# Kernel optimization log

Hardware: AMD Instinct MI355X
Metric: run time of the kernel (lower is better)

The kernel has to match this reference:

```python
import jax, jax.numpy as jnp
import numpy as np
import math

HEAD_DIM = 64
NQ = 24          # num query heads
NKV = 4          # num kv heads
HIDDEN = 1536
WINDOW = 256     # sliding window (layer_idx=0 -> active)
THETA = 10000.0
EPS = 1e-6


def _rope(x, cos, sin):
    # x: [B,S,H,D]; cos/sin: [S,1,D//2]  (broadcast over B and heads)
    xr = x.reshape(*x.shape[:-1], -1, 2)
    x1, x2 = xr[..., 0], xr[..., 1]
    r = jnp.stack([x1 * cos - x2 * sin, x2 * cos + x1 * sin], axis=-1)
    return r.reshape(x.shape)


def setup_inputs() -> dict:
    key = jax.random.key(0)
    k1, k2, k3 = jax.random.split(key, 3)
    B, S = 2, 2048
    x = jax.random.normal(k1, (B, S, HIDDEN), dtype=jnp.float32)
    norm_scale = jnp.ones((HIDDEN,), dtype=jnp.float32)             # RMSNorm scale
    w_qkv = jax.random.normal(k2, ((NQ + 2 * NKV) * HEAD_DIM, HIDDEN), dtype=jnp.float32) * 0.02
    w_out = jax.random.normal(k3, (HIDDEN, NQ * HEAD_DIM), dtype=jnp.float32) * 0.02
    return {"x": x, "norm_scale": norm_scale, "w_qkv": w_qkv, "w_out": w_out, "start_pos": 0}


def reference(x, norm_scale, w_qkv, w_out, start_pos):
    B, S, _ = x.shape
    # RMSNorm
    var = jnp.mean(x * x, axis=-1, keepdims=True)
    xn = x * jax.lax.rsqrt(var + EPS) * norm_scale
    # QKV projection (nn.Linear: x @ W^T)
    qkv = xn @ w_qkv.T
    qs, kvs = NQ * HEAD_DIM, NKV * HEAD_DIM
    q = qkv[..., :qs].reshape(B, S, NQ, HEAD_DIM)
    k = qkv[..., qs:qs + kvs].reshape(B, S, NKV, HEAD_DIM)
    v = qkv[..., qs + kvs:].reshape(B, S, NKV, HEAD_DIM)
    # RoPE
    inv_freq = 1.0 / (THETA ** (jnp.arange(0, HEAD_DIM, 2, dtype=jnp.float32) / HEAD_DIM))
    t = jnp.arange(start_pos, start_pos + S, dtype=jnp.float32)
    freqs = t[:, None] * inv_freq[None, :]                       # [S, D//2]
    cos, sin = jnp.cos(freqs)[:, None, :], jnp.sin(freqs)[:, None, :]
    q = _rope(q, cos, sin)
    k = _rope(k, cos, sin)
    # GQA: expand kv heads (repeat_interleave over head dim)
    rep = NQ // NKV
    k = jnp.repeat(k, rep, axis=2)
    v = jnp.repeat(v, rep, axis=2)
    # attention with causal + sliding-window mask
    scale = 1.0 / math.sqrt(HEAD_DIM)
    scores = jnp.einsum('bqhd,bkhd->bhqk', q * scale, k)        # [B,H,S,S]
    ipos = start_pos + jnp.arange(S)
    j = jnp.arange(S)
    mask = (j[None, :] > ipos[:, None]) | (j[None, :] < ipos[:, None] - WINDOW)
    scores = jnp.where(mask[None, None], -jnp.inf, scores)
    probs = jax.nn.softmax(scores, axis=-1)
    attn = jnp.einsum('bhqk,bkhd->bqhd', probs, v).reshape(B, S, NQ * HEAD_DIM)
    # output projection + residual
    return x + attn @ w_out.T
```

## Files before the change

kernel.cpp:

```cpp
#include <hip/hip_runtime.h>
#include <hip/hip_bf16.h>

typedef float f32x4 __attribute__((ext_vector_type(4)));
typedef short s16x8 __attribute__((ext_vector_type(8)));
typedef unsigned short u16;

#define B_ 2
#define S_ 2048
#define HID 1536
#define NQ_ 24
#define NKV_ 4
#define HD 64
#define NTOK (B_*S_)
#define QKVN ((NQ_+2*NKV_)*HD)
#define ROPE_BLOCKS ((NTOK*28*32)/256)
#define VT_BLOCKS (B_*NKV_*(S_/64))

#define LDS_FENCE() asm volatile("" ::: "memory")

#define WAITBAR(n) asm volatile("s_waitcnt vmcnt(" #n ")\n\ts_barrier" ::: "memory")
#define RAWBAR()   asm volatile("s_barrier" ::: "memory")

__device__ __forceinline__ float bf2f(u16 u) {
  unsigned int x = ((unsigned int)u) << 16;
  float f; __builtin_memcpy(&f, &x, 4); return f;
}
__device__ __forceinline__ u16 f2bf(float f) {
  unsigned int u; __builtin_memcpy(&u, &f, 4);
  u += 0x7fffu + ((u >> 16) & 1u);
  return (u16)(u >> 16);
}
__device__ __forceinline__ unsigned long long pk4bf(float a, float b, float c, float d) {
  __hip_bfloat162 x = __float22bfloat162_rn(make_float2(a, b));
  __hip_bfloat162 y = __float22bfloat162_rn(make_float2(c, d));
  unsigned int xi, yi;
  __builtin_memcpy(&xi, &x, 4);
  __builtin_memcpy(&yi, &y, 4);
  return (unsigned long long)xi | ((unsigned long long)yi << 32);
}

__global__ __launch_bounds__(256) void k_cvt2(const float* __restrict__ s0, int n0q,
                                              const float* __restrict__ s1, int n1q,
                                              u16* __restrict__ dst) {
  int i = blockIdx.x * 256 + threadIdx.x;
  if (i >= n0q + n1q) return;
  const float* src = (i < n0q) ? s0 : s1;
  int j = (i < n0q) ? i : i - n0q;
  f32x4 v = ((const f32x4*)src)[j];
  *(unsigned long long*)(dst + (size_t)i*4) = pk4bf(v[0], v[1], v[2], v[3]);
}

__global__ __launch_bounds__(384) void k_rmsnorm(const float* __restrict__ x,
                                                 const float* __restrict__ g,
                                                 u16* __restrict__ xn) {
  int row = blockIdx.x;
  int t = threadIdx.x;
  f32x4 v = ((const f32x4*)(x + (size_t)row * HID))[t];
  float ss = v[0]*v[0] + v[1]*v[1] + v[2]*v[2] + v[3]*v[3];
#pragma unroll
  for (int off = 1; off < 64; off <<= 1) ss += __shfl_xor(ss, off);
  __shared__ float red[6];
  if ((t & 63) == 0) red[t >> 6] = ss;
  __syncthreads();
  float tot = red[0] + red[1] + red[2] + red[3] + red[4] + red[5];
  float rs = rsqrtf(tot * (1.f/HID) + 1e-6f);
  f32x4 gv = ((const f32x4*)g)[t];
  ((unsigned long long*)(xn + (size_t)row * HID))[t] =
      pk4bf(v[0]*rs*gv[0], v[1]*rs*gv[1], v[2]*rs*gv[2], v[3]*rs*gv[3]);
}

template <bool F32OUT>
__global__ __launch_bounds__(256) void k_gemm_bt(const u16* __restrict__ A,
                                                 const u16* __restrict__ W,
                                                 void* __restrict__ Cv,
                                                 const float* __restrict__ resid,
                                                 int N, int K) {
  __shared__ __align__(16) u16 As0[128*64], Bs0[64*64];
  __shared__ __align__(16) u16 As1[128*64], Bs1[64*64];
  int lin = blockIdx.x;
  int xcd = lin & 7, loc = lin >> 3;
  int mloc = loc & 3, nloc = loc >> 2;
  int m0 = (xcd*4 + mloc) * 128, n0 = nloc * 64;
  int tid = threadIdx.x;
  int w = tid >> 6, l = tid & 63;
  int wr = w >> 1, wc = w & 1;
  int c = l & 15, g = l >> 4;
  f32x4 acc[4][2] = {};
  int r8 = l >> 3;
  int sslot = (l & 7) ^ r8;
  const u16* Ag = A + (size_t)(m0 + w*32 + r8)*K + sslot*8;
  const u16* Wg = W + (size_t)(n0 + w*16 + r8)*K + sslot*8;

#define STAGE(dA, dB, k0) do {                                                          \
  _Pragma("unroll")                                                                     \
  for (int i = 0; i < 4; i++)                                                           \
    __builtin_amdgcn_global_load_lds(                                                   \
        (const __attribute__((address_space(1))) void*)(Ag + (size_t)(i*8)*K + (k0)),   \
        (__attribute__((address_space(3))) void*)(dA + (w*32 + i*8)*64), 16, 0, 0);     \
  _Pragma("unroll")                                                                     \
  for (int i = 0; i < 2; i++)                                                           \
    __builtin_amdgcn_global_load_lds(                                                   \
        (const __attribute__((address_space(1))) void*)(Wg + (size_t)(i*8)*K + (k0)),   \
        (__attribute__((address_space(3))) void*)(dB + (w*16 + i*8)*64), 16, 0, 0);     \
  } while (0)

#define COMPUTE(sA, sB) do {                                                            \
  _Pragma("unroll")                                                                     \
  for (int ks = 0; ks < 2; ks++) {                                                      \
    s16x8 af[4], bq[2];                                                                 \
    int sl = ((ks*4 + g) ^ (c & 7)) * 8;                                                \
    _Pragma("unroll")                                                                   \
    for (int mt = 0; mt < 4; mt++)                                                      \
      af[mt] = *(const s16x8*)(sA + (wr*64 + mt*16 + c)*64 + sl);                       \
    _Pragma("unroll")                                                                   \
    for (int nt = 0; nt < 2; nt++)                                                      \
      bq[nt] = *(const s16x8*)(sB + (wc*32 + nt*16 + c)*64 + sl);                       \
    _Pragma("unroll")                                                                   \
    for (int mt = 0; mt < 4; mt++)                                                      \
      _Pragma("unroll")                                                                 \
      for (int nt = 0; nt < 2; nt++)                                                    \
        acc[mt][nt] = __builtin_amdgcn_mfma_f32_16x16x32_bf16(af[mt], bq[nt],           \
                                                              acc[mt][nt], 0, 0, 0);    \
  } } while (0)

  const int NT = K >> 6;
  STAGE(As0, Bs0, 0);
  STAGE(As1, Bs1, 64);
  WAITBAR(6);
  for (int t = 0; t + 2 < NT; t += 2) {
    COMPUTE(As0, Bs0);
    RAWBAR();
    STAGE(As0, Bs0, (t+2)*64);
    WAITBAR(6);
    COMPUTE(As1, Bs1);
    RAWBAR();
    if (t + 3 < NT) {
      STAGE(As1, Bs1, (t+3)*64);
      WAITBAR(6);
    } else {
      WAITBAR(0);
    }
  }
  COMPUTE(As0, Bs0);
  WAITBAR(0);
  COMPUTE(As1, Bs1);
#undef STAGE
#undef COMPUTE

#pragma unroll
  for (int mt = 0; mt < 4; mt++)
#pragma unroll
    for (int nt = 0; nt < 2; nt++)
#pragma unroll
      for (int r = 0; r < 4; r++) {
        int m = m0 + wr*64 + mt*16 + g*4 + r;
        int n = n0 + wc*32 + nt*16 + c;
        size_t off = (size_t)m*N + n;
        float vv = acc[mt][nt][r];
        if (F32OUT) {
          ((float*)Cv)[off] = vv + resid[off];
        } else {
          ((u16*)Cv)[off] = f2bf(vv);
        }
      }
}

__global__ __launch_bounds__(256) void k_rope_vt(const u16* __restrict__ qkv,
                                                 u16* __restrict__ q,
                                                 u16* __restrict__ k,
                                                 u16* __restrict__ vt,
                                                 const int* __restrict__ spp) {
  __shared__ u16 tile[64][65];
  int bid = blockIdx.x;
  if (bid < ROPE_BLOCKS) {
    int idx = bid * 256 + threadIdx.x;
    int p = idx & 31;
    int h = (idx >> 5) % 28;
    int tok = idx / 896;
    int s = tok & (S_ - 1);
    int b = tok >> 11;
    float t = (float)(spp[0] + s);
    float inv = exp2f((float)p * -0.41524101186f);
    float fr = t * inv;
    float sn, cs;
    sincosf(fr, &sn, &cs);
    int col = (h < NQ_) ? h*64 + 2*p : HID + (h - NQ_)*64 + 2*p;
    unsigned int pr = *(const unsigned int*)(qkv + (size_t)tok*QKVN + col);
    float x1 = bf2f((u16)(pr & 0xffff));
    float x2 = bf2f((u16)(pr >> 16));
    float y1 = x1*cs - x2*sn;
    float y2 = x2*cs + x1*sn;
    unsigned int outp = (unsigned int)f2bf(y1) | ((unsigned int)f2bf(y2) << 16);
    if (h < NQ_) {
      *(unsigned int*)(q + (((size_t)(b*NQ_ + h))*S_ + s)*64 + 2*p) = outp;
    } else {
      *(unsigned int*)(k + (((size_t)(b*NKV_ + (h - NQ_)))*S_ + s)*64 + 2*p) = outp;
    }
  } else {
    int blk = bid - ROPE_BLOCKS;
    int st = blk & 31;
    int hk = (blk >> 5) & 3;
    int b = blk >> 7;
    int s0 = st * 64;
#pragma unroll
    for (int i = 0; i < 16; i++) {
      int ii = threadIdx.x + i*256;
      int r = ii >> 6, cc = ii & 63;
      tile[r][cc] = qkv[((size_t)(b*S_) + s0 + r)*QKVN + (NQ_+NKV_)*64 + hk*64 + cc];
    }
    __syncthreads();
#pragma unroll
    for (int i = 0; i < 16; i++) {
      int ii = threadIdx.x + i*256;
      int d = ii >> 6, s = ii & 63;
      vt[((size_t)(b*NKV_ + hk)*64 + d)*S_ + s0 + s] = tile[s][d];
    }
  }
}

__global__ __launch_bounds__(64, 3) void k_attn(const u16* __restrict__ q,
                                                const u16* __restrict__ k,
                                                const u16* __restrict__ vt,
                                                u16* __restrict__ ao,
                                                const int* __restrict__ spp) {
  __shared__ __align__(16) u16 Pt[32*72];
  int lin = blockIdx.x;
  int xcd = lin & 7, loc = lin >> 3;
  int qb = loc & 63;
  int bh = xcd * 6 + (loc >> 6);
  int h = bh % NQ_;
  int b = bh / NQ_;
  int q0 = qb * 32;
  int hk = h / (NQ_/NKV_);
  int l = threadIdx.x;
  int c = l & 15, g = l >> 4;
  int sp = spp[0];
  const u16* qptr = q + ((size_t)(b*NQ_ + h))*S_*64;
  const u16* kptr = k + ((size_t)(b*NKV_ + hk))*S_*64;
  const u16* vptr = vt + ((size_t)(b*NKV_ + hk))*64*S_;

  s16x8 qf[2][2];
#pragma unroll
  for (int qt = 0; qt < 2; qt++)
#pragma unroll
    for (int ks = 0; ks < 2; ks++)
      qf[qt][ks] = *(const s16x8*)(qptr + (size_t)(q0 + qt*16 + c)*64 + ks*32 + g*8);

  f32x4 o[4][2] = {};
  float m_run[2], l_run[2];
#pragma unroll
  for (int i = 0; i < 2; i++) { m_run[i] = -1e30f; l_run[i] = 0.f; }

  int lo = sp + q0 - 256; if (lo < 0) lo = 0;
  int hi = sp + q0 + 31;  if (hi > S_ - 1) hi = S_ - 1;
  int kt0 = lo >> 6, kt1 = hi >> 6;

  s16x8 kf[4][2];
#pragma unroll
  for (int km = 0; km < 4; km++)
#pragma unroll
    for (int ks = 0; ks < 2; ks++)
      kf[km][ks] = *(const s16x8*)(kptr + (size_t)(kt0*64 + km*16 + c)*64 + ks*32 + g*8);

  for (int kt = kt0; kt <= kt1; kt++) {
    s16x8 vf[2][4];
#pragma unroll
    for (int ks = 0; ks < 2; ks++)
#pragma unroll
      for (int dt = 0; dt < 4; dt++)
        vf[ks][dt] = *(const s16x8*)(vptr + (size_t)(dt*16 + c)*S_ + kt*64 + ks*32 + g*8);

    bool full = (kt*64 + 63 <= sp + q0) && (kt*64 >= sp + q0 - 225);
#pragma unroll
    for (int qt = 0; qt < 2; qt++) {
      f32x4 sa[4];
      __builtin_amdgcn_s_setprio(1);
#pragma unroll
      for (int km = 0; km < 4; km++) {
        f32x4 z = {};
        z = __builtin_amdgcn_mfma_f32_16x16x32_bf16(kf[km][0], qf[qt][0], z, 0, 0, 0);
        sa[km] = __builtin_amdgcn_mfma_f32_16x16x32_bf16(kf[km][1], qf[qt][1], z, 0, 0, 0);
      }
      __builtin_amdgcn_s_setprio(0);
      if (qt == 1 && kt < kt1) {
#pragma unroll
        for (int km = 0; km < 4; km++)
#pragma unroll
          for (int ks = 0; ks < 2; ks++)
            kf[km][ks] = *(const s16x8*)(kptr + (size_t)((kt+1)*64 + km*16 + c)*64 + ks*32 + g*8);
      }
      float mx = -1e30f;
      if (full) {
#pragma unroll
        for (int km = 0; km < 4; km++)
#pragma unroll
          for (int r = 0; r < 4; r++) {
            float sv = sa[km][r] * 0.125f;
            sa[km][r] = sv;
            mx = fmaxf(mx, sv);
          }
      } else {
        int pos = sp + q0 + qt*16 + c;
#pragma unroll
        for (int km = 0; km < 4; km++)
#pragma unroll
          for (int r = 0; r < 4; r++) {
            int key = kt*64 + km*16 + g*4 + r;
            float sv = sa[km][r] * 0.125f;
            sv = ((unsigned)(pos - key) <= 256u) ? sv : -1e30f;
            sa[km][r] = sv;
            mx = fmaxf(mx, sv);
          }
      }
      mx = fmaxf(mx, __shfl_xor(mx, 16));
      mx = fmaxf(mx, __shfl_xor(mx, 32));
      float mnew = fmaxf(m_run[qt], mx);
      float alpha = __expf(m_run[qt] - mnew);
      m_run[qt] = mnew;
      float rsum = 0.f;
#pragma unroll
      for (int km = 0; km < 4; km++) {
        float p0 = __expf(sa[km][0] - mnew);
        float p1 = __expf(sa[km][1] - mnew);
        float p2 = __expf(sa[km][2] - mnew);
        float p3 = __expf(sa[km][3] - mnew);
        rsum += p0 + p1 + p2 + p3;
        *(unsigned long long*)(Pt + (qt*16 + c)*72 + km*16 + g*4) = pk4bf(p0, p1, p2, p3);
      }
      rsum += __shfl_xor(rsum, 16);
      rsum += __shfl_xor(rsum, 32);
      l_run[qt] = l_run[qt]*alpha + rsum;
#pragma unroll
      for (int dt = 0; dt < 4; dt++) {
        o[dt][qt][0] *= alpha; o[dt][qt][1] *= alpha;
        o[dt][qt][2] *= alpha; o[dt][qt][3] *= alpha;
      }
    }
    LDS_FENCE();
    __builtin_amdgcn_s_setprio(1);
#pragma unroll
    for (int ks = 0; ks < 2; ks++)
#pragma unroll
      for (int qt = 0; qt < 2; qt++) {
        s16x8 pf = *(const s16x8*)(Pt + (qt*16 + c)*72 + ks*32 + g*8);
#pragma unroll
        for (int dt = 0; dt < 4; dt++)
          o[dt][qt] = __builtin_amdgcn_mfma_f32_16x16x32_bf16(vf[ks][dt], pf, o[dt][qt], 0, 0, 0);
      }
    __builtin_amdgcn_s_setprio(0);
    LDS_FENCE();
  }
#pragma unroll
  for (int qt = 0; qt < 2; qt++) {
    float inv = 1.f / l_run[qt];
    int qi = q0 + qt*16 + c;
    u16* row = ao + ((size_t)(b*S_) + qi)*HID + h*64;
#pragma unroll
    for (int dt = 0; dt < 4; dt++)
      *(unsigned long long*)(row + dt*16 + g*4) =
          pk4bf(o[dt][qt][0]*inv, o[dt][qt][1]*inv, o[dt][qt][2]*inv, o[dt][qt][3]*inv);
  }
}

extern "C" void kernel_launch(void* const* d_in, const int* in_sizes, int n_in,
                              void* d_out, int out_size, void* d_ws, size_t ws_size,
                              hipStream_t stream) {
  const float* x_f32    = (const float*)d_in[0];
  const float* g_f32    = (const float*)d_in[1];
  const float* wqkv_f32 = (const float*)d_in[2];
  const float* wout_f32 = (const float*)d_in[3];
  const int*   spp      = (const int*)d_in[4];
  char* ws = (char*)d_ws;
  u16* wqkvb = (u16*)(ws);
  u16* woutb = (u16*)(ws + 6291456);
  u16* xn    = (u16*)(ws + 11010048);
  u16* qkv   = (u16*)(ws + 23592960);
  u16* qbuf  = (u16*)(ws + 40370176);
  u16* kbuf  = (u16*)(ws + 52953088);
  u16* vtb   = (u16*)(ws + 55050240);
  u16* attn  = xn;

  const int nwq4 = QKVN*HID/4, nwo4 = HID*HID/4;
  k_cvt2<<<(nwq4 + nwo4 + 255)/256, 256, 0, stream>>>(wqkv_f32, nwq4, wout_f32, nwo4, wqkvb);
  k_rmsnorm<<<NTOK, 384, 0, stream>>>(x_f32, g_f32, xn);
  k_gemm_bt<false><<<32*(QKVN/64), 256, 0, stream>>>(xn, wqkvb, qkv, nullptr, QKVN, HID);
  k_rope_vt<<<ROPE_BLOCKS + VT_BLOCKS, 256, 0, stream>>>(qkv, qbuf, kbuf, vtb, spp);
  k_attn<<<B_*NQ_*(S_/32), 64, 0, stream>>>(qbuf, kbuf, vtb, attn, spp);
  k_gemm_bt<true><<<32*(HID/64), 256, 0, stream>>>(attn, woutb, d_out, x_f32, HID, HID);
}
```

Measured before the change: 208.7 us.

## Merge setup kernels and precompute RoPE cos/sin table for vectorized rope

Weight conversion, RMSNorm and a new cos/sin table computation now run as one setup kernel, which removes a launch. The RoPE kernel reads precomputed cos/sin pairs from the table instead of calling sincosf per element, and each thread handles two rotation pairs with 64-bit loads and stores. The table is stored temporarily in the output buffer, which is later overwritten by the final GEMM. RMSNorm now uses 256-thread blocks with two vectors per thread for the first 192 threads.

```diff
diff --git a/kernel.cpp b/kernel.cpp
--- a/kernel.cpp
+++ b/kernel.cpp
@@ -13,7 +13,13 @@
 #define HD 64
 #define NTOK (B_*S_)
 #define QKVN ((NQ_+2*NKV_)*HD)
-#define ROPE_BLOCKS ((NTOK*28*32)/256)
+
+#define CVT_BLKS  ((QKVN*HID + HID*HID)/4/256)
+#define RMS_BLKS  NTOK
+#define TAB_BLKS  (S_*32/256)
+#define SETUP_BLKS (CVT_BLKS + RMS_BLKS + TAB_BLKS)
+
+#define ROPE2_BLOCKS ((NTOK*28*16)/256)
 #define VT_BLOCKS (B_*NKV_*(S_/64))
 
 #define LDS_FENCE() asm volatile("" ::: "memory")
@@ -39,34 +45,54 @@
   return (unsigned long long)xi | ((unsigned long long)yi << 32);
 }
 
-__global__ __launch_bounds__(256) void k_cvt2(const float* __restrict__ s0, int n0q,
-                                              const float* __restrict__ s1, int n1q,
-                                              u16* __restrict__ dst) {
-  int i = blockIdx.x * 256 + threadIdx.x;
-  if (i >= n0q + n1q) return;
-  const float* src = (i < n0q) ? s0 : s1;
-  int j = (i < n0q) ? i : i - n0q;
-  f32x4 v = ((const f32x4*)src)[j];
-  *(unsigned long long*)(dst + (size_t)i*4) = pk4bf(v[0], v[1], v[2], v[3]);
-}
-
-__global__ __launch_bounds__(384) void k_rmsnorm(const float* __restrict__ x,
-                                                 const float* __restrict__ g,
-                                                 u16* __restrict__ xn) {
-  int row = blockIdx.x;
-  int t = threadIdx.x;
-  f32x4 v = ((const f32x4*)(x + (size_t)row * HID))[t];
-  float ss = v[0]*v[0] + v[1]*v[1] + v[2]*v[2] + v[3]*v[3];
-#pragma unroll
-  for (int off = 1; off < 64; off <<= 1) ss += __shfl_xor(ss, off);
-  __shared__ float red[6];
-  if ((t & 63) == 0) red[t >> 6] = ss;
-  __syncthreads();
-  float tot = red[0] + red[1] + red[2] + red[3] + red[4] + red[5];
-  float rs = rsqrtf(tot * (1.f/HID) + 1e-6f);
-  f32x4 gv = ((const f32x4*)g)[t];
-  ((unsigned long long*)(xn + (size_t)row * HID))[t] =
-      pk4bf(v[0]*rs*gv[0], v[1]*rs*gv[1], v[2]*rs*gv[2], v[3]*rs*gv[3]);
+__global__ __launch_bounds__(256) void k_setup(const float* __restrict__ x,
+                                               const float* __restrict__ g,
+                                               const float* __restrict__ wq,
+                                               const float* __restrict__ wo,
+                                               u16* __restrict__ wb,
+                                               u16* __restrict__ xn,
+                                               float2* __restrict__ tab,
+                                               const int* __restrict__ spp) {
+  int bid = blockIdx.x, tid = threadIdx.x;
+  if (bid < CVT_BLKS) {
+    int i = bid * 256 + tid;
+    const int n0q = QKVN*HID/4;
+    const float* src = (i < n0q) ? wq : wo;
+    int j = (i < n0q) ? i : i - n0q;
+    f32x4 v = ((const f32x4*)src)[j];
+    *(unsigned long long*)(wb + (size_t)i*4) = pk4bf(v[0], v[1], v[2], v[3]);
+  } else if (bid < CVT_BLKS + RMS_BLKS) {
+    int row = bid - CVT_BLKS;
+    const f32x4* xr = (const f32x4*)(x + (size_t)row * HID);
+    f32x4 v0 = {}, v1 = {};
+    float ss = 0.f;
+    if (tid < 192) {
+      v0 = xr[2*tid]; v1 = xr[2*tid + 1];
+      ss = v0[0]*v0[0] + v0[1]*v0[1] + v0[2]*v0[2] + v0[3]*v0[3]
+         + v1[0]*v1[0] + v1[1]*v1[1] + v1[2]*v1[2] + v1[3]*v1[3];
+    }
+#pragma unroll
+    for (int off = 1; off < 64; off <<= 1) ss += __shfl_xor(ss, off);
+    __shared__ float red[4];
+    if ((tid & 63) == 0) red[tid >> 6] = ss;
+    __syncthreads();
+    float rs = rsqrtf((red[0] + red[1] + red[2] + red[3]) * (1.f/HID) + 1e-6f);
+    if (tid < 192) {
+      const f32x4* gr = (const f32x4*)g;
+      f32x4 g0 = gr[2*tid], g1 = gr[2*tid + 1];
+      unsigned long long* out = (unsigned long long*)(xn + (size_t)row * HID);
+      out[2*tid]     = pk4bf(v0[0]*rs*g0[0], v0[1]*rs*g0[1], v0[2]*rs*g0[2], v0[3]*rs*g0[3]);
+      out[2*tid + 1] = pk4bf(v1[0]*rs*g1[0], v1[1]*rs*g1[1], v1[2]*rs*g1[2], v1[3]*rs*g1[3]);
+    }
+  } else {
+    int i = (bid - CVT_BLKS - RMS_BLKS) * 256 + tid;
+    int s = i >> 5, p = i & 31;
+    float t = (float)(spp[0] + s);
+    float inv = exp2f((float)p * -0.41524101186f);
+    float sn, cs;
+    sincosf(t * inv, &sn, &cs);
+    tab[i] = make_float2(cs, sn);
+  }
 }
 
 template <bool F32OUT>
@@ -169,35 +195,33 @@
                                                  u16* __restrict__ q,
                                                  u16* __restrict__ k,
                                                  u16* __restrict__ vt,
-                                                 const int* __restrict__ spp) {
+                                                 const float2* __restrict__ tab) {
   __shared__ u16 tile[64][65];
   int bid = blockIdx.x;
-  if (bid < ROPE_BLOCKS) {
+  if (bid < ROPE2_BLOCKS) {
     int idx = bid * 256 + threadIdx.x;
-    int p = idx & 31;
-    int h = (idx >> 5) % 28;
-    int tok = idx / 896;
+    int j = idx & 15;
+    int h = (idx >> 4) % 28;
+    int tok = idx / 448;
     int s = tok & (S_ - 1);
     int b = tok >> 11;
-    float t = (float)(spp[0] + s);
-    float inv = exp2f((float)p * -0.41524101186f);
-    float fr = t * inv;
-    float sn, cs;
-    sincosf(fr, &sn, &cs);
-    int col = (h < NQ_) ? h*64 + 2*p : HID + (h - NQ_)*64 + 2*p;
-    unsigned int pr = *(const unsigned int*)(qkv + (size_t)tok*QKVN + col);
-    float x1 = bf2f((u16)(pr & 0xffff));
-    float x2 = bf2f((u16)(pr >> 16));
-    float y1 = x1*cs - x2*sn;
-    float y2 = x2*cs + x1*sn;
-    unsigned int outp = (unsigned int)f2bf(y1) | ((unsigned int)f2bf(y2) << 16);
+    f32x4 cs = *(const f32x4*)(tab + (size_t)s*32 + 2*j);
+    int col = (h < NQ_) ? h*64 + 4*j : HID + (h - NQ_)*64 + 4*j;
+    unsigned long long pr = *(const unsigned long long*)(qkv + (size_t)tok*QKVN + col);
+    float x1a = bf2f((u16)pr),         x2a = bf2f((u16)(pr >> 16));
+    float x1b = bf2f((u16)(pr >> 32)), x2b = bf2f((u16)(pr >> 48));
+    float ya1 = x1a*cs[0] - x2a*cs[1];
+    float ya2 = x2a*cs[0] + x1a*cs[1];
+    float yb1 = x1b*cs[2] - x2b*cs[3];
+    float yb2 = x2b*cs[2] + x1b*cs[3];
+    unsigned long long outp = pk4bf(ya1, ya2, yb1, yb2);
     if (h < NQ_) {
-      *(unsigned int*)(q + (((size_t)(b*NQ_ + h))*S_ + s)*64 + 2*p) = outp;
+      *(unsigned long long*)(q + (((size_t)(b*NQ_ + h))*S_ + s)*64 + 4*j) = outp;
     } else {
-      *(unsigned int*)(k + (((size_t)(b*NKV_ + (h - NQ_)))*S_ + s)*64 + 2*p) = outp;
+      *(unsigned long long*)(k + (((size_t)(b*NKV_ + (h - NQ_)))*S_ + s)*64 + 4*j) = outp;
     }
   } else {
-    int blk = bid - ROPE_BLOCKS;
+    int blk = bid - ROPE2_BLOCKS;
     int st = blk & 31;
     int hk = (blk >> 5) & 3;
     int b = blk >> 7;
@@ -379,12 +403,13 @@
   u16* kbuf  = (u16*)(ws + 52953088);
   u16* vtb   = (u16*)(ws + 55050240);
   u16* attn  = xn;
-
-  const int nwq4 = QKVN*HID/4, nwo4 = HID*HID/4;
-  k_cvt2<<<(nwq4 + nwo4 + 255)/256, 256, 0, stream>>>(wqkv_f32, nwq4, wout_f32, nwo4, wqkvb);
-  k_rmsnorm<<<NTOK, 384, 0, stream>>>(x_f32, g_f32, xn);
+  float2* tab = (float2*)d_out;
+
+  k_setup<<<SETUP_BLKS, 256, 0, stream>>>(x_f32, g_f32, wqkv_f32, wout_f32,
+                                          wqkvb, xn, tab, spp);
   k_gemm_bt<false><<<32*(QKVN/64), 256, 0, stream>>>(xn, wqkvb, qkv, nullptr, QKVN, HID);
-  k_rope_vt<<<ROPE_BLOCKS + VT_BLOCKS, 256, 0, stream>>>(qkv, qbuf, kbuf, vtb, spp);
+  k_rope_vt<<<ROPE2_BLOCKS + VT_BLOCKS, 256, 0, stream>>>(qkv, qbuf, kbuf, vtb,
+                                                          (const float2*)tab);
   k_attn<<<B_*NQ_*(S_/32), 64, 0, stream>>>(qbuf, kbuf, vtb, attn, spp);
   k_gemm_bt<true><<<32*(HID/64), 256, 0, stream>>>(attn, woutb, d_out, x_f32, HID, HID);
 }
```

Result: faster. 202.9 us (-2.7%).
